# Kernel tuning notes

Measured on AMD Instinct MI355X. Metric: run time of the kernel, lower is better.

Reference implementation:

```python
import jax, jax.numpy as jnp
import numpy as np

INPUT_DIM = 256
UNITS = 256
BATCH = 65536


def _glorot(key, shape):
    fan_in, fan_out = shape
    limit = np.sqrt(6.0 / (fan_in + fan_out)).astype(np.float32)
    return jax.random.uniform(key, shape, jnp.float32, -limit, limit)


def setup_inputs() -> dict:
    key = jax.random.key(0)
    ks = jax.random.split(key, 8)
    d = {
        "inputs": jax.random.normal(ks[0], (BATCH, INPUT_DIM), jnp.float32),
        "h_prev": jax.random.normal(ks[1], (BATCH, UNITS), jnp.float32),
        "c_prev": jax.random.normal(ks[2], (BATCH, UNITS), jnp.float32),
        "W_f": _glorot(ks[3], (INPUT_DIM + UNITS, UNITS)),
        "W_i": _glorot(ks[4], (INPUT_DIM + UNITS, UNITS)),
        "W_c": _glorot(ks[5], (INPUT_DIM + UNITS, UNITS)),
        "W_o": _glorot(ks[6], (INPUT_DIM + UNITS, UNITS)),
        "b_f": jnp.zeros((UNITS,), jnp.float32),
        "b_i": jnp.zeros((UNITS,), jnp.float32),
        "b_c": jnp.zeros((UNITS,), jnp.float32),
        "b_o": jnp.zeros((UNITS,), jnp.float32),
    }
    return d


def reference(inputs, h_prev, c_prev, W_f, W_i, W_c, W_o, b_f, b_i, b_c, b_o):
    # z: [B, input_dim + units]
    z = jnp.concatenate([inputs, h_prev], axis=-1)
    f = jax.nn.sigmoid(z @ W_f + b_f)
    i = jax.nn.sigmoid(z @ W_i + b_i)
    c_tilde = jnp.tanh(z @ W_c + b_c)
    c = f * c_prev + i * c_tilde
    o = jax.nn.sigmoid(z @ W_o + b_o)
    h = o * jnp.tanh(c)
    return h, c
```

## Files before the change

kernel.cpp:

```cpp
#include <hip/hip_runtime.h>
#include <hip/hip_bf16.h>
#include <stdint.h>

#define BATCH   65536
#define UNITS   256
#define NCHUNK  8
#define ROWP    68
#define GSZ     (64 * ROWP)
#define SMEM_BYTES 34816

using f32x16 = __attribute__((ext_vector_type(16))) float;
using bf16x8 = __attribute__((ext_vector_type(8))) short;

__device__ __forceinline__ short f2bf(float f) {
  union { float f; unsigned u; } v; v.f = f;
  unsigned r = v.u + 0x7FFFu + ((v.u >> 16) & 1u);
  return (short)(r >> 16);
}
__device__ __forceinline__ float bf2f(short s) {
  union { float f; unsigned u; } v; v.u = ((unsigned)(unsigned short)s) << 16;
  return v.f;
}
__device__ __forceinline__ unsigned pk2(float a, float b) {
  union { __hip_bfloat162 h; unsigned u; } cv;
  cv.h = __float22bfloat162_rn(make_float2(a, b));
  return cv.u;
}
__device__ __forceinline__ bf16x8 cvt8(float4 a, float4 b) {
  union { unsigned u[4]; bf16x8 v; } r;
  r.u[0] = pk2(a.x, a.y); r.u[1] = pk2(a.z, a.w);
  r.u[2] = pk2(b.x, b.y); r.u[3] = pk2(b.z, b.w);
  return r.v;
}

#define LOG2E 1.4426950408889634f
__device__ __forceinline__ float fast_sigmoid(float x) {
  return __builtin_amdgcn_rcpf(1.f + __builtin_amdgcn_exp2f(x * -LOG2E));
}
__device__ __forceinline__ float fast_tanh(float x) {
  return 2.f * __builtin_amdgcn_rcpf(1.f + __builtin_amdgcn_exp2f(x * (-2.f * LOG2E))) - 1.f;
}

#define BAR() do { asm volatile("s_waitcnt lgkmcnt(0)" ::: "memory"); \
                   __builtin_amdgcn_s_barrier(); } while (0)

__global__ void cvt_weights(const float* __restrict__ Wf, const float* __restrict__ Wi,
                            const float* __restrict__ Wc, const float* __restrict__ Wo,
                            short* __restrict__ Wt) {
  int idx = blockIdx.x * 256 + threadIdx.x;
  int g   = idx >> 17;
  int k   = (idx >> 8) & 511;
  int col = idx & 255;
  const float* W = (g == 0) ? Wf : (g == 1) ? Wi : (g == 2) ? Wc : Wo;
  float val = W[k * 256 + col];
  int nb = col >> 6, n = col & 63;
  int c = k >> 6, kg = (k >> 3) & 7, k8 = k & 7;
  int out = ((((g * 4 + nb) * 8 + c) * 8 + kg) * 64 + n) * 8 + k8;
  Wt[out] = f2bf(val);
}

__global__ __launch_bounds__(256, 3) void lstm_fused(
    const float* __restrict__ x, const float* __restrict__ hprev,
    const float* __restrict__ cprev, const short* __restrict__ Wt,
    const float* __restrict__ bfp, const float* __restrict__ bip,
    const float* __restrict__ bcp, const float* __restrict__ bop,
    float* __restrict__ hout, float* __restrict__ cout)
{
  extern __shared__ __align__(16) char smem[];
  const int tid  = threadIdx.x;
  const int g    = tid >> 6;
  const int lane = tid & 63;
  const int la   = lane & 31;
  const int hh   = lane >> 5;

  int bid = blockIdx.x;
  int wg  = (bid & 7) * 512 + (bid >> 3);
  const int m0 = (wg >> 2) * 64;
  const int nb = wg & 3;
  const int n0 = nb * 64;

  const short* Bbase = Wt + ((size_t)(g * 4 + nb)) * 32768 + hh * 512 + la * 8;

  f32x16 acc[2][2] = {};
  bf16x8 breg[8];
  float4 vA[2][4];

  const int arow  = tid >> 2;
  const int q     = tid & 3;
  const int slotW = (arow ^ (q << 2)) & 63;

  auto ldA = [&](int c, float4* v) {
    const float* base = (c < 4) ? x : hprev;
    const float* rowp = base + (size_t)(m0 + arow) * 256 + (c & 3) * 64;
    v[0] = *(const float4*)(rowp + q * 8);
    v[1] = *(const float4*)(rowp + q * 8 + 4);
    v[2] = *(const float4*)(rowp + (q + 4) * 8);
    v[3] = *(const float4*)(rowp + (q + 4) * 8 + 4);
  };
  auto wrA = [&](int buf, const float4* v) {
    char* Ab = smem + buf * 8192;
    *(bf16x8*)(Ab + q * 1024 + slotW * 16)       = cvt8(v[0], v[1]);
    *(bf16x8*)(Ab + (q + 4) * 1024 + slotW * 16) = cvt8(v[2], v[3]);
  };
  auto loadB = [&](int c, int ks) {
    const short* Bc = Bbase + (size_t)c * 4096 + ks * 1024;
    breg[2 * ks]     = *(const bf16x8*)(Bc);
    breg[2 * ks + 1] = *(const bf16x8*)(Bc + 256);
  };

  const int ccol = tid & 63;
  const int rg   = tid >> 6;
  const size_t gbase = (size_t)(m0 + rg * 16) * 256 + n0 + ccol;

  ldA(0, vA[0]);
  ldA(1, vA[1]);
  wrA(0, vA[0]);
#pragma unroll
  for (int ks = 0; ks < 4; ++ks) loadB(0, ks);
  float cp[16];
#pragma unroll
  for (int j = 0; j < 16; ++j) cp[j] = cprev[gbase + (size_t)j * 256];
  ldA(2, vA[0]);
  BAR();

  int buf = 0;
#pragma unroll
  for (int c = 0; c < NCHUNK; ++c) {
    if (c + 1 < NCHUNK) wrA(buf ^ 1, vA[(c + 1) & 1]);
    if (c + 3 < NCHUNK) ldA(c + 3, vA[(c + 3) & 1]);
    const char*  Ab = smem + buf * 8192;
    const short* Bn = Bbase + (size_t)((c + 1) & 7) * 4096;
#pragma unroll
    for (int ks = 0; ks < 4; ++ks) {
      const int kg   = 2 * ks + hh;
      const int slot = la ^ ((kg & 3) << 2);
      const int off  = kg * 1024 + slot * 16;
      bf16x8 a0 = *(const bf16x8*)(Ab + off);
      bf16x8 a1 = *(const bf16x8*)(Ab + off + 512);
      acc[0][0] = __builtin_amdgcn_mfma_f32_32x32x16_bf16(a0, breg[2*ks],   acc[0][0], 0, 0, 0);
      acc[0][1] = __builtin_amdgcn_mfma_f32_32x32x16_bf16(a0, breg[2*ks+1], acc[0][1], 0, 0, 0);
      acc[1][0] = __builtin_amdgcn_mfma_f32_32x32x16_bf16(a1, breg[2*ks],   acc[1][0], 0, 0, 0);
      acc[1][1] = __builtin_amdgcn_mfma_f32_32x32x16_bf16(a1, breg[2*ks+1], acc[1][1], 0, 0, 0);
      breg[2*ks]     = *(const bf16x8*)(Bn + ks * 1024);
      breg[2*ks + 1] = *(const bf16x8*)(Bn + ks * 1024 + 256);
    }
    BAR();
    buf ^= 1;
  }

  const float* bptr = (g == 0) ? bfp : (g == 1) ? bip : (g == 2) ? bcp : bop;
  const float bias0 = bptr[n0 + la];
  const float bias1 = bptr[n0 + 32 + la];
  short* G = (short*)smem;
#pragma unroll
  for (int mi = 0; mi < 2; ++mi)
#pragma unroll
    for (int ni = 0; ni < 2; ++ni) {
      const float bias = ni ? bias1 : bias0;
      const int   col  = la + ni * 32;
#pragma unroll
      for (int rq = 0; rq < 4; ++rq) {
        const int row0 = rq * 8 + 4 * hh + mi * 32;
        float t[4];
#pragma unroll
        for (int e = 0; e < 4; ++e) {
          float vv = acc[mi][ni][rq * 4 + e] + bias;
          t[e] = (g == 2) ? fast_tanh(vv) : fast_sigmoid(vv);
        }
        uint2 u; u.x = pk2(t[0], t[1]); u.y = pk2(t[2], t[3]);
        *(uint2*)(G + g * GSZ + col * ROWP + row0) = u;
      }
    }
  BAR();

  {
    const short* Gp = G + ccol * ROWP + rg * 16;
    bf16x8 gf[4][2];
#pragma unroll
    for (int gg = 0; gg < 4; ++gg) {
      gf[gg][0] = *(const bf16x8*)(Gp + gg * GSZ);
      gf[gg][1] = *(const bf16x8*)(Gp + gg * GSZ + 8);
    }
#pragma unroll
    for (int j = 0; j < 16; ++j) {
      float fg = bf2f(gf[0][j >> 3][j & 7]);
      float ig = bf2f(gf[1][j >> 3][j & 7]);
      float cg = bf2f(gf[2][j >> 3][j & 7]);
      float og = bf2f(gf[3][j >> 3][j & 7]);
      float cnew = fg * cp[j] + ig * cg;
      float hnew = og * fast_tanh(cnew);
      hout[gbase + (size_t)j * 256] = hnew;
      cout[gbase + (size_t)j * 256] = cnew;
    }
  }
}

extern "C" void kernel_launch(void* const* d_in, const int* in_sizes, int n_in,
                              void* d_out, int out_size, void* d_ws, size_t ws_size,
                              hipStream_t stream) {
  const float* x     = (const float*)d_in[0];
  const float* hprev = (const float*)d_in[1];
  const float* cprev = (const float*)d_in[2];
  const float* Wf    = (const float*)d_in[3];
  const float* Wi    = (const float*)d_in[4];
  const float* Wc    = (const float*)d_in[5];
  const float* Wo    = (const float*)d_in[6];
  const float* bfp   = (const float*)d_in[7];
  const float* bip   = (const float*)d_in[8];
  const float* bcp   = (const float*)d_in[9];
  const float* bop   = (const float*)d_in[10];
  float* out = (float*)d_out;
  short* Wt  = (short*)d_ws;

  cvt_weights<<<2048, 256, 0, stream>>>(Wf, Wi, Wc, Wo, Wt);

  lstm_fused<<<dim3(4096), dim3(256), SMEM_BYTES, stream>>>(
      x, hprev, cprev, Wt, bfp, bip, bcp, bop,
      out, out + (size_t)BATCH * UNITS);
}
```

Before: 156.2 us.

## Stage weights into LDS via direct global-to-LDS loads with finer K chunks

Weight tiles are no longer held in registers. They are copied straight into double-buffered LDS with global_load_lds, and the K loop is split into 16 chunks of 32 instead of 8 chunks of 64. Explicit vmcnt waits order the loads, and occupancy is raised from 3 to 4 blocks per SIMD via launch bounds. The goal is to cut register pressure and hide global-load latency through asynchronous staging. In exchange there are more barriers per tile, extra LDS traffic for the B operand, and a weight layout that changes to match.

Measured after the change: 143.5 us. 8.1% less time.

```diff
diff --git a/kernel.cpp b/kernel.cpp
--- a/kernel.cpp
+++ b/kernel.cpp
@@ -4,10 +4,10 @@
 
 #define BATCH   65536
 #define UNITS   256
-#define NCHUNK  8
+#define NCH     16
 #define ROWP    68
 #define GSZ     (64 * ROWP)
-#define SMEM_BYTES 34816
+#define SMEM_BYTES 40960
 
 using f32x16 = __attribute__((ext_vector_type(16))) float;
 using bf16x8 = __attribute__((ext_vector_type(8))) short;
@@ -32,7 +32,6 @@
   r.u[2] = pk2(b.x, b.y); r.u[3] = pk2(b.z, b.w);
   return r.v;
 }
-
 #define LOG2E 1.4426950408889634f
 __device__ __forceinline__ float fast_sigmoid(float x) {
   return __builtin_amdgcn_rcpf(1.f + __builtin_amdgcn_exp2f(x * -LOG2E));
@@ -43,6 +42,14 @@
 
 #define BAR() do { asm volatile("s_waitcnt lgkmcnt(0)" ::: "memory"); \
                    __builtin_amdgcn_s_barrier(); } while (0)
+#define WAITV(n) asm volatile("s_waitcnt vmcnt(" #n ")" ::: "memory")
+
+__device__ __forceinline__ void gload_lds16(const void* gsrc, void* ldst) {
+  __builtin_amdgcn_global_load_lds(
+      (const __attribute__((address_space(1))) void*)gsrc,
+      (__attribute__((address_space(3))) void*)ldst,
+      16, 0, 0);
+}
 
 __global__ void cvt_weights(const float* __restrict__ Wf, const float* __restrict__ Wi,
                             const float* __restrict__ Wc, const float* __restrict__ Wo,
@@ -54,12 +61,12 @@
   const float* W = (g == 0) ? Wf : (g == 1) ? Wi : (g == 2) ? Wc : Wo;
   float val = W[k * 256 + col];
   int nb = col >> 6, n = col & 63;
-  int c = k >> 6, kg = (k >> 3) & 7, k8 = k & 7;
-  int out = ((((g * 4 + nb) * 8 + c) * 8 + kg) * 64 + n) * 8 + k8;
+  int kg = k >> 3, k8 = k & 7;
+  int out = (((g * 4 + nb) * 64 + kg) * 64 + n) * 8 + k8;
   Wt[out] = f2bf(val);
 }
 
-__global__ __launch_bounds__(256, 3) void lstm_fused(
+__global__ __launch_bounds__(256, 4) void lstm_fused(
     const float* __restrict__ x, const float* __restrict__ hprev,
     const float* __restrict__ cprev, const short* __restrict__ Wt,
     const float* __restrict__ bfp, const float* __restrict__ bip,
@@ -79,78 +86,80 @@
   const int nb = wg & 3;
   const int n0 = nb * 64;
 
-  const short* Bbase = Wt + ((size_t)(g * 4 + nb)) * 32768 + hh * 512 + la * 8;
+  const short* WtG = Wt + ((size_t)(g * 4 + nb)) * 32768;
 
   f32x16 acc[2][2] = {};
-  bf16x8 breg[8];
-  float4 vA[2][4];
+  float4 vA[2][2];
 
   const int arow  = tid >> 2;
   const int q     = tid & 3;
-  const int slotW = (arow ^ (q << 2)) & 63;
-
-  auto ldA = [&](int c, float4* v) {
-    const float* base = (c < 4) ? x : hprev;
-    const float* rowp = base + (size_t)(m0 + arow) * 256 + (c & 3) * 64;
-    v[0] = *(const float4*)(rowp + q * 8);
-    v[1] = *(const float4*)(rowp + q * 8 + 4);
-    v[2] = *(const float4*)(rowp + (q + 4) * 8);
-    v[3] = *(const float4*)(rowp + (q + 4) * 8 + 4);
-  };
-  auto wrA = [&](int buf, const float4* v) {
-    char* Ab = smem + buf * 8192;
-    *(bf16x8*)(Ab + q * 1024 + slotW * 16)       = cvt8(v[0], v[1]);
-    *(bf16x8*)(Ab + (q + 4) * 1024 + slotW * 16) = cvt8(v[2], v[3]);
-  };
-  auto loadB = [&](int c, int ks) {
-    const short* Bc = Bbase + (size_t)c * 4096 + ks * 1024;
-    breg[2 * ks]     = *(const bf16x8*)(Bc);
-    breg[2 * ks + 1] = *(const bf16x8*)(Bc + 256);
-  };
+  const int slotW = arow ^ (q << 2);
+
+  char* Abase = smem;
+  char* Bbase = smem + 8192;
+
+  auto ldA = [&](int c) {
+    const float* base = (c < 8) ? x : hprev;
+    const float* rowp = base + (size_t)(m0 + arow) * 256 + (c & 7) * 32 + q * 8;
+    vA[c & 1][0] = *(const float4*)(rowp);
+    vA[c & 1][1] = *(const float4*)(rowp + 4);
+  };
+  auto wrA = [&](int c) {
+    char* Ab = Abase + (c & 1) * 4096;
+    *(bf16x8*)(Ab + q * 1024 + slotW * 16) = cvt8(vA[c & 1][0], vA[c & 1][1]);
+  };
+  auto stageB = [&](int c) {
+    char* ldst = Bbase + (c & 1) * 16384 + g * 4096;
+    const short* gs = WtG + c * 2048 + lane * 8;
+#pragma unroll
+    for (int i = 0; i < 4; ++i)
+      gload_lds16(gs + i * 512, ldst + i * 1024);
+  };
+  auto compute = [&](int c) {
+    const char* Ab = Abase + (c & 1) * 4096;
+    const char* Bl = Bbase + (c & 1) * 16384 + g * 4096;
+#pragma unroll
+    for (int ks = 0; ks < 2; ++ks) {
+      const int kg = 2 * ks + hh;
+      const int ao = kg * 1024 + ((la ^ (kg << 2)) * 16);
+      bf16x8 a0 = *(const bf16x8*)(Ab + ao);
+      bf16x8 a1 = *(const bf16x8*)(Ab + ao + 512);
+      bf16x8 b0 = *(const bf16x8*)(Bl + kg * 1024 + la * 16);
+      bf16x8 b1 = *(const bf16x8*)(Bl + kg * 1024 + la * 16 + 512);
+      acc[0][0] = __builtin_amdgcn_mfma_f32_32x32x16_bf16(a0, b0, acc[0][0], 0, 0, 0);
+      acc[0][1] = __builtin_amdgcn_mfma_f32_32x32x16_bf16(a0, b1, acc[0][1], 0, 0, 0);
+      acc[1][0] = __builtin_amdgcn_mfma_f32_32x32x16_bf16(a1, b0, acc[1][0], 0, 0, 0);
+      acc[1][1] = __builtin_amdgcn_mfma_f32_32x32x16_bf16(a1, b1, acc[1][1], 0, 0, 0);
+    }
+  };
+
+  ldA(0); stageB(0); ldA(1); stageB(1);
+  wrA(0);
+
+#pragma unroll
+  for (int c = 0; c < NCH; ++c) {
+    if (c + 2 < NCH) ldA(c + 2);
+    if (c < NCH - 2)      WAITV(8);
+    else if (c == NCH - 2) WAITV(6);
+    else                   WAITV(0);
+    BAR();
+    if (c + 1 < NCH) wrA(c + 1);
+    compute(c);
+    __builtin_amdgcn_sched_barrier(0);
+    if (c + 2 < NCH) stageB(c + 2);
+  }
 
   const int ccol = tid & 63;
   const int rg   = tid >> 6;
   const size_t gbase = (size_t)(m0 + rg * 16) * 256 + n0 + ccol;
-
-  ldA(0, vA[0]);
-  ldA(1, vA[1]);
-  wrA(0, vA[0]);
-#pragma unroll
-  for (int ks = 0; ks < 4; ++ks) loadB(0, ks);
   float cp[16];
 #pragma unroll
   for (int j = 0; j < 16; ++j) cp[j] = cprev[gbase + (size_t)j * 256];
-  ldA(2, vA[0]);
-  BAR();
-
-  int buf = 0;
-#pragma unroll
-  for (int c = 0; c < NCHUNK; ++c) {
-    if (c + 1 < NCHUNK) wrA(buf ^ 1, vA[(c + 1) & 1]);
-    if (c + 3 < NCHUNK) ldA(c + 3, vA[(c + 3) & 1]);
-    const char*  Ab = smem + buf * 8192;
-    const short* Bn = Bbase + (size_t)((c + 1) & 7) * 4096;
-#pragma unroll
-    for (int ks = 0; ks < 4; ++ks) {
-      const int kg   = 2 * ks + hh;
-      const int slot = la ^ ((kg & 3) << 2);
-      const int off  = kg * 1024 + slot * 16;
-      bf16x8 a0 = *(const bf16x8*)(Ab + off);
-      bf16x8 a1 = *(const bf16x8*)(Ab + off + 512);
-      acc[0][0] = __builtin_amdgcn_mfma_f32_32x32x16_bf16(a0, breg[2*ks],   acc[0][0], 0, 0, 0);
-      acc[0][1] = __builtin_amdgcn_mfma_f32_32x32x16_bf16(a0, breg[2*ks+1], acc[0][1], 0, 0, 0);
-      acc[1][0] = __builtin_amdgcn_mfma_f32_32x32x16_bf16(a1, breg[2*ks],   acc[1][0], 0, 0, 0);
-      acc[1][1] = __builtin_amdgcn_mfma_f32_32x32x16_bf16(a1, breg[2*ks+1], acc[1][1], 0, 0, 0);
-      breg[2*ks]     = *(const bf16x8*)(Bn + ks * 1024);
-      breg[2*ks + 1] = *(const bf16x8*)(Bn + ks * 1024 + 256);
-    }
-    BAR();
-    buf ^= 1;
-  }
 
   const float* bptr = (g == 0) ? bfp : (g == 1) ? bip : (g == 2) ? bcp : bop;
   const float bias0 = bptr[n0 + la];
   const float bias1 = bptr[n0 + 32 + la];
+  BAR();
   short* G = (short*)smem;
 #pragma unroll
   for (int mi = 0; mi < 2; ++mi)
```
